# Kernel optimization log

Hardware: AMD Instinct MI355X
Metric: run time of the kernel (lower is better)

The kernel has to match this reference:

```python
import jax, jax.numpy as jnp
import numpy as np

BSZ, IN_DIM, OUT_DIM = 512, 1024, 2048
M_AND = 5        # Anderson memory (self.m)
BETA = 1.0
LAM = 1e-4
ALPHA = 1.0
TOL = 1e-5
MAX_ITER = 50
M_MON = 1.0      # monotonicity parameter of MONSingleFc


def _multiply(A, B, z):
    # MONSingleFc.multiply: (1-m)z - z A^T A + z B^T - z B
    Az = z @ A.T
    return (1.0 - M_MON) * z - Az @ A + z @ B.T - z @ B


def _relu(z):
    return jnp.maximum(z, 0.0)


def _single_it(A, B, z, bias):
    zn = _multiply(A, B, z)
    zn = (1.0 - ALPHA) * z + ALPHA * (zn + bias)
    zn = _relu(zn)
    err = jnp.linalg.norm(zn - z) / (1e-6 + jnp.linalg.norm(zn))
    return zn, err


def _anderson_solve(A, B, bias):
    bsz, d = bias.shape
    dt = bias.dtype
    Z = jnp.zeros((bsz, M_AND, d), dt)
    F = jnp.zeros((bsz, M_AND, d), dt)
    z0 = jnp.zeros((bsz, d), dt)
    f0, _ = _single_it(A, B, z0, bias)
    F = F.at[:, 0].set(f0)
    Z = Z.at[:, 1].set(f0)
    f1, _ = _single_it(A, B, f0, bias)
    F = F.at[:, 1].set(f1)
    eye = jnp.eye(M_AND, dtype=dt)

    def cond(s):
        Z, F, it, err = s
        return (it < MAX_ITER) & (err > TOL)

    def body(s):
        Z, F, it, _ = s
        n = jnp.minimum(M_AND, it)
        mask = jnp.arange(M_AND) < n                         # active Anderson slots
        # For it < m the unused slots of Z and F are still zero, so G = F - Z
        # has zero rows there and GGt's Frobenius norm matches the :n slice.
        G = F - Z                                            # (bsz, m, d)
        GGt = jnp.einsum('bmd,bnd->bmn', G, G)
        nrm = jnp.linalg.norm(GGt.reshape(GGt.shape[0], -1), axis=-1)
        GGt = GGt / (nrm[:, None, None] + 1e-6)
        pair = mask[:, None] & mask[None, :]
        # identity padding on inactive slots keeps the solve well-posed and
        # yields alpha = 0 there, equivalent to slicing [:n+1, :n+1].
        Hb = jnp.where(pair, GGt + LAM * eye, eye)
        mk = mask.astype(dt)
        H = jnp.zeros((bsz, M_AND + 1, M_AND + 1), dt)
        H = H.at[:, 0, 1:].set(mk).at[:, 1:, 0].set(mk).at[:, 1:, 1:].set(Hb)
        y = jnp.zeros((bsz, M_AND + 1, 1), dt).at[:, 0, 0].set(1.0)
        alpha = jnp.linalg.solve(H, y)[:, 1:, 0]             # (bsz, m)
        z_new = BETA * jnp.einsum('bm,bmd->bd', alpha, F) \
              + (1.0 - BETA) * jnp.einsum('bm,bmd->bd', alpha, Z)
        slot = it % M_AND
        Z = Z.at[:, slot].set(z_new)
        zo, err = _single_it(A, B, z_new, bias)
        F = F.at[:, slot].set(zo)
        return Z, F, it + 1, err

    Z, F, it, err = jax.lax.while_loop(
        cond, body, (Z, F, jnp.array(2, jnp.int32), jnp.array(jnp.inf, dt)))
    slot = (it - 1) % M_AND
    return Z[:, slot]


def setup_inputs():
    key = jax.random.key(0)
    kx, ka, kb, kw, kub = jax.random.split(key, 5)
    s = 1.0 / np.sqrt(OUT_DIM).astype(np.float32)
    x = jax.random.normal(kx, (BSZ, IN_DIM), jnp.float32)
    # scaled so ||W|| < 1 -> forward-backward splitting converges (trained MON regime)
    A = 0.3 * s * jax.random.normal(ka, (OUT_DIM, OUT_DIM), jnp.float32)
    B = 0.1 * s * jax.random.normal(kb, (OUT_DIM, OUT_DIM), jnp.float32)
    U_W = (1.0 / np.sqrt(IN_DIM).astype(np.float32)) * jax.random.normal(kw, (OUT_DIM, IN_DIM), jnp.float32)
    U_b = 0.01 * jax.random.normal(kub, (OUT_DIM,), jnp.float32)
    return {"x": x, "A": A, "B": B, "U_W": U_W, "U_b": U_b}


def reference(x, A, B, U_W, U_b):
    bias = x @ U_W.T + U_b                       # linear_module.bias(x)
    z_star = _anderson_solve(A, B, bias)         # equilibrium (no-grad in torch)
    zn = _relu(_multiply(A, B, z_star) + bias)   # final full step: nonlin(linear(x, z*))
    return zn
```

## Files before the change

kernel.cpp:

```cpp
#include <hip/hip_runtime.h>
#include <hip/hip_bf16.h>
#include <math.h>

#define BSZ      512
#define IN_DIM   1024
#define OUT_DIM  2048
#define M_AND    5
#define LAM      1e-4f
#define TOL      1e-5f
#define MAX_ITER 50
#define SPLIT_IT 24
#define NBLK     256

typedef __bf16 bf16x8 __attribute__((ext_vector_type(8)));
typedef float  f32x4  __attribute__((ext_vector_type(4)));
typedef unsigned short u16x8 __attribute__((ext_vector_type(8)));
typedef unsigned short u16x4 __attribute__((ext_vector_type(4)));
typedef __hip_bfloat16 bf16;

#define GAS __attribute__((address_space(1)))
#define LAS __attribute__((address_space(3)))

#define S_WAITCNT_VMCNT(N) asm volatile("s_waitcnt vmcnt(" #N ")" ::: "memory")

union BU { bf16 b; unsigned short u; };

__device__ __forceinline__ float bf2f(unsigned short u) {
    union { unsigned int i; float f; } c; c.i = (unsigned int)u << 16; return c.f;
}
__device__ __forceinline__ unsigned short f2bf(float f) {
    BU t; t.b = __float2bfloat16(f); return t.u;
}

static constexpr size_t BIAS_B = 0;
static constexpr size_t F_B    = BIAS_B + (size_t)BSZ * OUT_DIM * 4;
static constexpr size_t G_B    = F_B    + (size_t)BSZ * M_AND * OUT_DIM * 4;
static constexpr size_t ZH_B   = G_B    + (size_t)BSZ * M_AND * OUT_DIM * 2;
static constexpr size_t ZL_B   = ZH_B   + (size_t)BSZ * OUT_DIM * 2;
static constexpr size_t XH_B   = ZL_B   + (size_t)BSZ * OUT_DIM * 2;
static constexpr size_t XL_B   = XH_B   + (size_t)BSZ * IN_DIM * 2;
static constexpr size_t UH_B   = XL_B   + (size_t)BSZ * IN_DIM * 2;
static constexpr size_t UL_B   = UH_B   + (size_t)OUT_DIM * IN_DIM * 2;
static constexpr size_t AT_B   = UL_B   + (size_t)OUT_DIM * IN_DIM * 2;
static constexpr size_t WT_B   = AT_B   + (size_t)OUT_DIM * OUT_DIM * 2;
static constexpr size_t RED_B  = WT_B   + (size_t)OUT_DIM * OUT_DIM * 2;
static constexpr size_t BAR_B  = RED_B  + 512;
static constexpr size_t CTR_B  = BAR_B  + 64;
static constexpr size_t FLAG_B = CTR_B  + 256;
static constexpr size_t FSLOT_B = FLAG_B + 16;
static constexpr size_t CTRL_SZ = 512 + 64 + 256 + 16 + 16;

template<int ROUNDS>
__device__ __forceinline__ void stage_tile(const void* __restrict__ g0, int row_bytes,
                                           void* l0, int tid)
{
    #pragma unroll
    for (int q = 0; q < ROUNDS; ++q) {
        const int D   = q * 4096 + tid * 16;
        const int r   = D >> 7;
        const int cb  = D & 127;
        const int scb = cb ^ ((r & 7) << 4);
        const char* gsrc = (const char*)g0 + (size_t)r * row_bytes + scb;
        char* ldst = (char*)l0 + q * 4096 + (tid >> 6) * 1024;
        __builtin_amdgcn_global_load_lds((const GAS void*)gsrc, (LAS void*)ldst, 16, 0, 0);
    }
}

__device__ __forceinline__ bf16x8 read_frag(const void* tile, int row, int cb)
{
    return *(const bf16x8*)((const char*)tile + row * 128 + (cb ^ ((row & 7) << 4)));
}

__device__ __forceinline__ void gsync(unsigned int* bar)
{
    __syncthreads();
    if (threadIdx.x == 0) {
        __threadfence();
        const unsigned int g =
            __hip_atomic_load(&bar[1], __ATOMIC_ACQUIRE, __HIP_MEMORY_SCOPE_AGENT);
        const unsigned int a =
            __hip_atomic_fetch_add(&bar[0], 1u, __ATOMIC_ACQ_REL, __HIP_MEMORY_SCOPE_AGENT);
        if (a == NBLK - 1) {
            __hip_atomic_store(&bar[0], 0u, __ATOMIC_RELAXED, __HIP_MEMORY_SCOPE_AGENT);
            __hip_atomic_fetch_add(&bar[1], 1u, __ATOMIC_RELEASE, __HIP_MEMORY_SCOPE_AGENT);
        } else {
            while (__hip_atomic_load(&bar[1], __ATOMIC_ACQUIRE, __HIP_MEMORY_SCOPE_AGENT) == g)
                __builtin_amdgcn_s_sleep(1);
        }
        __threadfence();
    }
    __syncthreads();
}

__global__ __launch_bounds__(256)
void conv_hilo(const float* __restrict__ src, bf16* __restrict__ h, bf16* __restrict__ l)
{
    const size_t i4 = ((size_t)blockIdx.x * 256 + threadIdx.x) * 4;
    const float4 v = *(const float4*)&src[i4];
    const float vv[4] = {v.x, v.y, v.z, v.w};
    union { short4 s4; unsigned short u[4]; } ph, pl;
    #pragma unroll
    for (int j = 0; j < 4; ++j) {
        ph.u[j] = f2bf(vv[j]);
        pl.u[j] = f2bf(vv[j] - bf2f(ph.u[j]));
    }
    *(short4*)((char*)h + i4 * 2) = ph.s4;
    *(short4*)((char*)l + i4 * 2) = pl.s4;
}

__global__ __launch_bounds__(256)
void prep_at(const float* __restrict__ A, bf16* __restrict__ At)
{
    __shared__ float t[64][65];
    const int tid = threadIdx.x;
    const int k0 = blockIdx.y * 64, c0 = blockIdx.x * 64;
    const int cc = tid & 63, rr = tid >> 6;
    #pragma unroll
    for (int q = 0; q < 16; ++q)
        t[rr + 4 * q][cc] = A[(size_t)(k0 + rr + 4 * q) * OUT_DIM + c0 + cc];
    __syncthreads();
    #pragma unroll
    for (int q = 0; q < 16; ++q)
        At[(size_t)(c0 + rr + 4 * q) * OUT_DIM + k0 + cc] = __float2bfloat16(t[cc][rr + 4 * q]);
}

__global__ __launch_bounds__(256)
void w_mfma(const bf16* __restrict__ At, const float* __restrict__ Bm, bf16* __restrict__ Wt)
{
    __shared__ __align__(16) bf16 lds[2][2][64 * 64];
    const int tid = threadIdx.x;
    const int lane = tid & 63, wid = tid >> 6;
    const int wy = wid >> 1, wx = wid & 1;

    int bb = blockIdx.x;
    int ti = (int)((sqrtf(8.f * bb + 1.f) - 1.f) * 0.5f);
    while ((ti + 1) * (ti + 2) / 2 <= bb) ++ti;
    while (ti * (ti + 1) / 2 > bb) --ti;
    const int tj = bb - ti * (ti + 1) / 2;
    const int r0 = ti * 64, c0 = tj * 64;
    const bool diag = (ti == tj);

    f32x4 acc[2][2];
    #pragma unroll
    for (int i = 0; i < 2; ++i)
        #pragma unroll
        for (int j = 0; j < 2; ++j) acc[i][j] = 0;

    stage_tile<2>(At + (size_t)r0 * OUT_DIM, OUT_DIM * 2, lds[0][0], tid);
    stage_tile<2>(At + (size_t)c0 * OUT_DIM, OUT_DIM * 2, lds[0][1], tid);
    __syncthreads();
    int cur = 0;
    for (int t = 0; t < 32; ++t) {
        if (t + 1 < 32) {
            const int kk = (t + 1) * 64;
            stage_tile<2>(At + (size_t)r0 * OUT_DIM + kk, OUT_DIM * 2, lds[cur ^ 1][0], tid);
            stage_tile<2>(At + (size_t)c0 * OUT_DIM + kk, OUT_DIM * 2, lds[cur ^ 1][1], tid);
        }
        const bf16* Ta = lds[cur][0];
        const bf16* Tb = lds[cur][1];
        #pragma unroll
        for (int kf = 0; kf < 2; ++kf) {
            const int cb = kf * 64 + (lane >> 4) * 16;
            bf16x8 bfr[2];
            #pragma unroll
            for (int nj = 0; nj < 2; ++nj)
                bfr[nj] = read_frag(Tb, wx * 32 + nj * 16 + (lane & 15), cb);
            #pragma unroll
            for (int mi = 0; mi < 2; ++mi) {
                bf16x8 afr = read_frag(Ta, wy * 32 + mi * 16 + (lane & 15), cb);
                #pragma unroll
                for (int nj = 0; nj < 2; ++nj)
                    acc[mi][nj] = __builtin_amdgcn_mfma_f32_16x16x32_bf16(afr, bfr[nj], acc[mi][nj], 0, 0, 0);
            }
        }
        __syncthreads();
        cur ^= 1;
    }

    #pragma unroll
    for (int mi = 0; mi < 2; ++mi) {
        const int rb = r0 + wy * 32 + mi * 16 + (lane >> 4) * 4;
        #pragma unroll
        for (int nj = 0; nj < 2; ++nj) {
            const int c = c0 + wx * 32 + nj * 16 + (lane & 15);
            const float4 bc = *(const float4*)&Bm[(size_t)c * OUT_DIM + rb];
            const float bcv[4] = {bc.x, bc.y, bc.z, bc.w};
            union { short4 s4; unsigned short u[4]; } p;
            #pragma unroll
            for (int g = 0; g < 4; ++g) {
                const float a = acc[mi][nj][g];
                const float brc = Bm[(size_t)(rb + g) * OUT_DIM + c];
                const float w = bcv[g] - brc - a;
                p.u[g] = f2bf(w);
                if (!diag) {
                    const float wm = brc - bcv[g] - a;
                    *((unsigned short*)Wt + (size_t)(rb + g) * OUT_DIM + c) = f2bf(wm);
                }
            }
            *(short4*)((char*)Wt + ((size_t)c * OUT_DIM + rb) * 2) = p.s4;
        }
    }
}

__global__ __launch_bounds__(256)
void bias_mfma(const bf16* __restrict__ xh, const bf16* __restrict__ xl,
               const bf16* __restrict__ uh, const bf16* __restrict__ ul,
               const float* __restrict__ Ub, float* __restrict__ bias,
               float* __restrict__ F, unsigned short* __restrict__ G,
               unsigned short* __restrict__ zh, unsigned short* __restrict__ zl)
{
    __shared__ __align__(16) bf16 lds[2][4][64 * 64];
    const int tid = threadIdx.x;
    const int lane = tid & 63, wid = tid >> 6;
    const int wy = wid >> 1, wx = wid & 1;
    const int m0 = blockIdx.y * 64, n0 = blockIdx.x * 64;

    f32x4 acc[2][2];
    #pragma unroll
    for (int i = 0; i < 2; ++i)
        #pragma unroll
        for (int j = 0; j < 2; ++j) acc[i][j] = 0;

    stage_tile<2>(xh + (size_t)m0 * IN_DIM, IN_DIM * 2, lds[0][0], tid);
    stage_tile<2>(xl + (size_t)m0 * IN_DIM, IN_DIM * 2, lds[0][1], tid);
    stage_tile<2>(uh + (size_t)n0 * IN_DIM, IN_DIM * 2, lds[0][2], tid);
    stage_tile<2>(ul + (size_t)n0 * IN_DIM, IN_DIM * 2, lds[0][3], tid);
    __syncthreads();
    int cur = 0;
    for (int t = 0; t < 16; ++t) {
        if (t + 1 < 16) {
            const int kk = (t + 1) * 64;
            stage_tile<2>(xh + (size_t)m0 * IN_DIM + kk, IN_DIM * 2, lds[cur ^ 1][0], tid);
            stage_tile<2>(xl + (size_t)m0 * IN_DIM + kk, IN_DIM * 2, lds[cur ^ 1][1], tid);
            stage_tile<2>(uh + (size_t)n0 * IN_DIM + kk, IN_DIM * 2, lds[cur ^ 1][2], tid);
            stage_tile<2>(ul + (size_t)n0 * IN_DIM + kk, IN_DIM * 2, lds[cur ^ 1][3], tid);
        }
        const bf16* Txh = lds[cur][0];
        const bf16* Txl = lds[cur][1];
        const bf16* Tuh = lds[cur][2];
        const bf16* Tul = lds[cur][3];
        #pragma unroll
        for (int kf = 0; kf < 2; ++kf) {
            const int cb = kf * 64 + (lane >> 4) * 16;
            bf16x8 bh[2], bl[2];
            #pragma unroll
            for (int nj = 0; nj < 2; ++nj) {
                const int br = wx * 32 + nj * 16 + (lane & 15);
                bh[nj] = read_frag(Tuh, br, cb);
                bl[nj] = read_frag(Tul, br, cb);
            }
            #pragma unroll
            for (int mi = 0; mi < 2; ++mi) {
                const int ar = wy * 32 + mi * 16 + (lane & 15);
                bf16x8 ah = read_frag(Txh, ar, cb);
                bf16x8 al = read_frag(Txl, ar, cb);
                #pragma unroll
                for (int nj = 0; nj < 2; ++nj) {
                    acc[mi][nj] = __builtin_amdgcn_mfma_f32_16x16x32_bf16(ah, bh[nj], acc[mi][nj], 0, 0, 0);
                    acc[mi][nj] = __builtin_amdgcn_mfma_f32_16x16x32_bf16(ah, bl[nj], acc[mi][nj], 0, 0, 0);
                    acc[mi][nj] = __builtin_amdgcn_mfma_f32_16x16x32_bf16(al, bh[nj], acc[mi][nj], 0, 0, 0);
                }
            }
        }
        __syncthreads();
        cur ^= 1;
    }

    #pragma unroll
    for (int mi = 0; mi < 2; ++mi) {
        const int mb = m0 + wy * 32 + mi * 16 + (lane >> 4) * 4;
        #pragma unroll
        for (int nj = 0; nj < 2; ++nj) {
            const int n = n0 + wx * 32 + nj * 16 + (lane & 15);
            const float ub = Ub[n];
            #pragma unroll
            for (int g = 0; g < 4; ++g) {
                const int m = mb + g;
                const size_t idx = (size_t)m * OUT_DIM + n;
                const float v = acc[mi][nj][g] + ub;
                bias[idx] = v;
                const float f = fmaxf(v, 0.f);
                F[((size_t)m * M_AND + 0) * OUT_DIM + n] = f;
                G[((size_t)m * M_AND + 0) * OUT_DIM + n] = f2bf(f);
                const unsigned short h = f2bf(f);
                zh[idx] = h;
                zl[idx] = f2bf(f - bf2f(h));
            }
        }
    }
}

template<bool DO_ERR>
__device__ __forceinline__ void iter_core(
    const int m0, const int n0, const int tid,
    const unsigned short* __restrict__ zh, const unsigned short* __restrict__ zl,
    const bf16* __restrict__ Wt, const float* __restrict__ bias,
    float* __restrict__ F, unsigned short* __restrict__ G,
    float* red, bf16* lds_buf, const int slot, const int it)
{
    const int lane = tid & 63, wid = tid >> 6;
    const int wy = wid >> 1, wx = wid & 1;
    #define BUFP(s,i) (lds_buf + ((s) * 3 + (i)) * 4096)

    f32x4 acc[2][2];
    #pragma unroll
    for (int i = 0; i < 2; ++i)
        #pragma unroll
        for (int j = 0; j < 2; ++j) acc[i][j] = 0;

    auto STAGE = [&](int s, int kk) {
        stage_tile<2>(zh + (size_t)m0 * OUT_DIM + kk, OUT_DIM * 2, BUFP(s, 0), tid);
        stage_tile<2>(zl + (size_t)m0 * OUT_DIM + kk, OUT_DIM * 2, BUFP(s, 1), tid);
        stage_tile<2>(Wt + (size_t)n0 * OUT_DIM + kk, OUT_DIM * 2, BUFP(s, 2), tid);
    };

    STAGE(0, 0);
    STAGE(1, 64);
    for (int t = 0; t < 32; ++t) {
        const int s = t % 3;
        if (t + 2 < 32) { S_WAITCNT_VMCNT(6); } else { S_WAITCNT_VMCNT(0); }
        __builtin_amdgcn_s_barrier();
        if (t + 2 < 32) STAGE((t + 2) % 3, (t + 2) * 64);
        const bf16* Th = BUFP(s, 0);
        const bf16* Tl = BUFP(s, 1);
        const bf16* Tw = BUFP(s, 2);
        #pragma unroll
        for (int kf = 0; kf < 2; ++kf) {
            const int cb = kf * 64 + (lane >> 4) * 16;
            bf16x8 bfr[2];
            #pragma unroll
            for (int nj = 0; nj < 2; ++nj)
                bfr[nj] = read_frag(Tw, wx * 32 + nj * 16 + (lane & 15), cb);
            #pragma unroll
            for (int mi = 0; mi < 2; ++mi) {
                const int rrow = wy * 32 + mi * 16 + (lane & 15);
                bf16x8 ah = read_frag(Th, rrow, cb);
                bf16x8 al = read_frag(Tl, rrow, cb);
                #pragma unroll
                for (int nj = 0; nj < 2; ++nj) {
                    acc[mi][nj] = __builtin_amdgcn_mfma_f32_16x16x32_bf16(ah, bfr[nj], acc[mi][nj], 0, 0, 0);
                    acc[mi][nj] = __builtin_amdgcn_mfma_f32_16x16x32_bf16(al, bfr[nj], acc[mi][nj], 0, 0, 0);
                }
            }
        }
    }
    #undef BUFP

    float lnum = 0.f, lden = 0.f;
    #pragma unroll
    for (int mi = 0; mi < 2; ++mi) {
        const int mb = m0 + wy * 32 + mi * 16 + (lane >> 4) * 4;
        #pragma unroll
        for (int nj = 0; nj < 2; ++nj) {
            const int n = n0 + wx * 32 + nj * 16 + (lane & 15);
            #pragma unroll
            for (int g = 0; g < 4; ++g) {
                const int m = mb + g;
                const size_t idx = (size_t)m * OUT_DIM + n;
                float v = acc[mi][nj][g] + bias[idx];
                v = fmaxf(v, 0.f);
                const float zc = bf2f(zh[idx]) + bf2f(zl[idx]);
                const float gg = v - zc;
                F[((size_t)m * M_AND + slot) * OUT_DIM + n] = v;
                G[((size_t)m * M_AND + slot) * OUT_DIM + n] = f2bf(gg);
                if (DO_ERR) { lnum += gg * gg; lden += v * v; }
            }
        }
    }

    if (DO_ERR) {
        #pragma unroll
        for (int off = 32; off; off >>= 1) {
            lnum += __shfl_down(lnum, off);
            lden += __shfl_down(lden, off);
        }
        __shared__ float swn[4], swd[4];
        if ((tid & 63) == 0) { swn[tid >> 6] = lnum; swd[tid >> 6] = lden; }
        __syncthreads();
        if (tid == 0) {
            atomicAdd(&red[2 * it],     swn[0] + swn[1] + swn[2] + swn[3]);
            atomicAdd(&red[2 * it + 1], swd[0] + swd[1] + swd[2] + swd[3]);
        }
    }
}

__device__ __forceinline__ void swz_mn(int bid, int& m0, int& n0)
{
    const int xcd = bid & 7, sl = bid >> 3;
    n0 = (xcd * 4 + (sl & 3)) * 64;
    m0 = (sl >> 2) * 64;
}

template<bool DO_ERR>
__global__ __launch_bounds__(256)
void iter_mfma(const unsigned short* __restrict__ zh, const unsigned short* __restrict__ zl,
               const bf16* __restrict__ Wt, const float* __restrict__ bias,
               float* __restrict__ F, unsigned short* __restrict__ G,
               float* red, unsigned int* ctr, int* flag, int* fslot, int slot, int it)
{
    if (((volatile int*)flag)[0]) return;
    __shared__ __align__(16) bf16 lds_buf[3 * 3 * 4096];
    int m0, n0;
    swz_mn(blockIdx.x, m0, n0);
    iter_core<DO_ERR>(m0, n0, threadIdx.x, zh, zl, Wt, bias, F, G, red, lds_buf, slot, it);
    if (DO_ERR && threadIdx.x == 0) {
        __threadfence();
        const unsigned int done = atomicAdd(&ctr[it], 1u);
        if (done == 256 - 1) {
            ((volatile int*)fslot)[0] = slot;
            const float num2 = ((volatile float*)red)[2 * it];
            const float den2 = ((volatile float*)red)[2 * it + 1];
            if (sqrtf(num2) <= TOL * (1e-6f + sqrtf(den2)))
                ((volatile int*)flag)[0] = 1;
        }
    }
}

__global__ __launch_bounds__(256)
void final_copy(const float* __restrict__ F, const int* __restrict__ fslot,
                float* __restrict__ out)
{
    const int s = ((volatile const int*)fslot)[0];
    const size_t i4 = ((size_t)blockIdx.x * 256 + threadIdx.x) * 4;
    const int m = (int)(i4 >> 11), n = (int)(i4 & 2047);
    *(float4*)&out[i4] = *(const float4*)&F[((size_t)m * M_AND + s) * OUT_DIM + n];
}

__global__ __launch_bounds__(512)
void anderson_kernel(const float* __restrict__ F, const unsigned short* __restrict__ G,
                     unsigned short* __restrict__ zh, unsigned short* __restrict__ zl,
                     int* flag, int it)
{
    if (((volatile int*)flag)[0]) return;
    const int b = blockIdx.x;
    const int tid = threadIdx.x;
    const int lane = tid & 63, wid = tid >> 6;
    const int n = (it < M_AND) ? it : M_AND;
    const int c0 = tid * 4;
    const unsigned short* Gb = G + (size_t)b * M_AND * OUT_DIM;
    const float* Fb = F + (size_t)b * M_AND * OUT_DIM;

    float g[M_AND][4];
    float4 f[M_AND];
    #pragma unroll
    for (int m = 0; m < M_AND; ++m) {
        f[m] = *(const float4*)(Fb + (size_t)m * OUT_DIM + c0);
        if (m < n) {
            const u16x4 gv = *(const u16x4*)(Gb + (size_t)m * OUT_DIM + c0);
            #pragma unroll
            for (int q = 0; q < 4; ++q) g[m][q] = bf2f(gv[q]);
        } else {
            #pragma unroll
            for (int q = 0; q < 4; ++q) g[m][q] = 0.f;
        }
    }

    float dots[15];
    {
        int p = 0;
        #pragma unroll
        for (int i = 0; i < M_AND; ++i)
            #pragma unroll
            for (int j = i; j < M_AND; ++j) {
                float s = 0.f;
                #pragma unroll
                for (int q = 0; q < 4; ++q) s += g[i][q] * g[j][q];
                dots[p++] = s;
            }
    }

    __shared__ float sred[15][8];
    #pragma unroll
    for (int p = 0; p < 15; ++p) {
        float v = dots[p];
        #pragma unroll
        for (int off = 32; off; off >>= 1) v += __shfl_xor(v, off);
        if (lane == 0) sred[p][wid] = v;
    }
    __syncthreads();

    __shared__ float s_alpha[M_AND];
    if (tid == 0) {
        float GGm[M_AND][M_AND];
        int p = 0;
        for (int i = 0; i < M_AND; ++i)
            for (int j = i; j < M_AND; ++j) {
                float v = 0.f;
                for (int w = 0; w < 8; ++w) v += sred[p][w];
                GGm[i][j] = v; GGm[j][i] = v; ++p;
            }
        float fro = 0.f;
        for (int i = 0; i < M_AND; ++i)
            for (int j = 0; j < M_AND; ++j) fro += GGm[i][j] * GGm[i][j];
        const float inv = 1.f / (sqrtf(fro) + 1e-6f);

        float Mm[M_AND][M_AND];
        for (int i = 0; i < n; ++i)
            for (int j = 0; j < n; ++j)
                Mm[i][j] = GGm[i][j] * inv + (i == j ? LAM : 0.f);

        float L[M_AND][M_AND];
        for (int i = 0; i < n; ++i)
            for (int j = 0; j <= i; ++j) {
                float s = Mm[i][j];
                for (int k = 0; k < j; ++k) s -= L[i][k] * L[j][k];
                L[i][j] = (i == j) ? sqrtf(fmaxf(s, 1e-20f)) : s / L[j][j];
            }
        float y[M_AND], u[M_AND];
        for (int i = 0; i < n; ++i) {
            float s = 1.f;
            for (int k = 0; k < i; ++k) s -= L[i][k] * y[k];
            y[i] = s / L[i][i];
        }
        for (int i = n - 1; i >= 0; --i) {
            float s = y[i];
            for (int k = i + 1; k < n; ++k) s -= L[k][i] * u[k];
            u[i] = s / L[i][i];
        }
        float su = 0.f;
        for (int i = 0; i < n; ++i) su += u[i];
        const float isu = 1.f / su;
        for (int m = 0; m < M_AND; ++m) s_alpha[m] = (m < n) ? u[m] * isu : 0.f;
    }
    __syncthreads();

    float z[4] = {};
    #pragma unroll
    for (int m = 0; m < M_AND; ++m) {
        if (m < n) {
            const float a = s_alpha[m];
            z[0] += a * f[m].x; z[1] += a * f[m].y;
            z[2] += a * f[m].z; z[3] += a * f[m].w;
        }
    }
    u16x4 hv, lv;
    #pragma unroll
    for (int q = 0; q < 4; ++q) {
        const unsigned short h = f2bf(z[q]);
        hv[q] = h;
        lv[q] = f2bf(z[q] - bf2f(h));
    }
    *(u16x4*)(zh + (size_t)b * OUT_DIM + c0) = hv;
    *(u16x4*)(zl + (size_t)b * OUT_DIM + c0) = lv;
}

__global__ __launch_bounds__(256)
void tail_loop(unsigned short* zh, unsigned short* zl,
               const bf16* __restrict__ Wt, const float* __restrict__ bias,
               float* F, unsigned short* G,
               float* red, unsigned int* bar, int* flag, int* fslot)
{
    if (((volatile int*)flag)[0]) return;
    __shared__ __align__(16) bf16 lds_buf[3 * 3 * 4096];
    __shared__ float sred2[2][2][15];
    __shared__ float s_alpha[2][M_AND];
    const int bid = blockIdx.x, tid = threadIdx.x;
    int m0, n0;
    swz_mn(bid, m0, n0);

    for (int it = SPLIT_IT; it < MAX_ITER; ++it) {
        {
            const int half = tid >> 7, lt = tid & 127;
            const int r = bid * 2 + half;
            const int wv = lt >> 6;
            const unsigned short* Gb = G + (size_t)r * M_AND * OUT_DIM;
            const float* Fb = F + (size_t)r * M_AND * OUT_DIM;
            const int c0 = lt * 16;

            float g[M_AND][16];
            #pragma unroll
            for (int m = 0; m < M_AND; ++m) {
                const u16x8 ga = *(const u16x8*)(Gb + (size_t)m * OUT_DIM + c0);
                const u16x8 gb2 = *(const u16x8*)(Gb + (size_t)m * OUT_DIM + c0 + 8);
                #pragma unroll
                for (int q = 0; q < 8; ++q) { g[m][q] = bf2f(ga[q]); g[m][8 + q] = bf2f(gb2[q]); }
            }
            {
                int p = 0;
                #pragma unroll
                for (int i = 0; i < M_AND; ++i)
                    #pragma unroll
                    for (int j = i; j < M_AND; ++j) {
                        float s = 0.f;
                        #pragma unroll
                        for (int q = 0; q < 16; ++q) s += g[i][q] * g[j][q];
                        float v = s;
                        #pragma unroll
                        for (int off = 32; off; off >>= 1) v += __shfl_xor(v, off);
                        if ((lt & 63) == 0) sred2[half][wv][p] = v;
                        ++p;
                    }
            }
            __syncthreads();
            if (lt == 0) {
                float GGm[M_AND][M_AND];
                int p = 0;
                for (int i = 0; i < M_AND; ++i)
                    for (int j = i; j < M_AND; ++j) {
                        const float v = sred2[half][0][p] + sred2[half][1][p];
                        GGm[i][j] = v; GGm[j][i] = v; ++p;
                    }
                float fro = 0.f;
                for (int i = 0; i < M_AND; ++i)
                    for (int j = 0; j < M_AND; ++j) fro += GGm[i][j] * GGm[i][j];
                const float inv = 1.f / (sqrtf(fro) + 1e-6f);
                float Mm[M_AND][M_AND];
                for (int i = 0; i < M_AND; ++i)
                    for (int j = 0; j < M_AND; ++j)
                        Mm[i][j] = GGm[i][j] * inv + (i == j ? LAM : 0.f);
                float L[M_AND][M_AND];
                for (int i = 0; i < M_AND; ++i)
                    for (int j = 0; j <= i; ++j) {
                        float s = Mm[i][j];
                        for (int k = 0; k < j; ++k) s -= L[i][k] * L[j][k];
                        L[i][j] = (i == j) ? sqrtf(fmaxf(s, 1e-20f)) : s / L[j][j];
                    }
                float y[M_AND], u[M_AND];
                for (int i = 0; i < M_AND; ++i) {
                    float s = 1.f;
                    for (int k = 0; k < i; ++k) s -= L[i][k] * y[k];
                    y[i] = s / L[i][i];
                }
                for (int i = M_AND - 1; i >= 0; --i) {
                    float s = y[i];
                    for (int k = i + 1; k < M_AND; ++k) s -= L[k][i] * u[k];
                    u[i] = s / L[i][i];
                }
                float su = 0.f;
                for (int i = 0; i < M_AND; ++i) su += u[i];
                const float isu = 1.f / su;
                for (int m = 0; m < M_AND; ++m) s_alpha[half][m] = u[m] * isu;
            }
            __syncthreads();
            float z[16] = {};
            for (int m = 0; m < M_AND; ++m) {
                const float a = s_alpha[half][m];
                #pragma unroll
                for (int q = 0; q < 4; ++q) {
                    const float4 fv = *(const float4*)(Fb + (size_t)m * OUT_DIM + c0 + q * 4);
                    z[q * 4 + 0] += a * fv.x; z[q * 4 + 1] += a * fv.y;
                    z[q * 4 + 2] += a * fv.z; z[q * 4 + 3] += a * fv.w;
                }
            }
            u16x8 hv[2], lv[2];
            #pragma unroll
            for (int q = 0; q < 16; ++q) {
                const unsigned short h = f2bf(z[q]);
                hv[q >> 3][q & 7] = h;
                lv[q >> 3][q & 7] = f2bf(z[q] - bf2f(h));
            }
            const size_t base = (size_t)r * OUT_DIM + c0;
            *(u16x8*)(zh + base)     = hv[0];
            *(u16x8*)(zh + base + 8) = hv[1];
            *(u16x8*)(zl + base)     = lv[0];
            *(u16x8*)(zl + base + 8) = lv[1];
        }
        gsync(bar);
        iter_core<true>(m0, n0, tid, zh, zl, Wt, bias, F, G, red, lds_buf, it % M_AND, it);
        gsync(bar);
        if (bid == 0 && tid == 0) ((volatile int*)fslot)[0] = it % M_AND;
        const float num2 = __hip_atomic_load(&red[2 * it], __ATOMIC_RELAXED, __HIP_MEMORY_SCOPE_AGENT);
        const float den2 = __hip_atomic_load(&red[2 * it + 1], __ATOMIC_RELAXED, __HIP_MEMORY_SCOPE_AGENT);
        if (sqrtf(num2) <= TOL * (1e-6f + sqrtf(den2))) break;
    }
}

extern "C" void kernel_launch(void* const* d_in, const int* in_sizes, int n_in,
                              void* d_out, int out_size, void* d_ws, size_t ws_size,
                              hipStream_t stream)
{
    const float* x  = (const float*)d_in[0];
    const float* A  = (const float*)d_in[1];
    const float* B  = (const float*)d_in[2];
    const float* UW = (const float*)d_in[3];
    const float* Ub = (const float*)d_in[4];
    float* out = (float*)d_out;
    char*  wsb = (char*)d_ws;

    float*          bias = (float*)(wsb + BIAS_B);
    float*          F    = (float*)(wsb + F_B);
    unsigned short* G    = (unsigned short*)(wsb + G_B);
    unsigned short* zh   = (unsigned short*)(wsb + ZH_B);
    unsigned short* zl   = (unsigned short*)(wsb + ZL_B);
    bf16*           xh   = (bf16*)(wsb + XH_B);
    bf16*           xl   = (bf16*)(wsb + XL_B);
    bf16*           uh   = (bf16*)(wsb + UH_B);
    bf16*           ul   = (bf16*)(wsb + UL_B);
    bf16*           At   = (bf16*)(wsb + AT_B);
    bf16*           Wt   = (bf16*)(wsb + WT_B);
    float*          red  = (float*)(wsb + RED_B);
    unsigned int*   bar  = (unsigned int*)(wsb + BAR_B);
    unsigned int*   ctr  = (unsigned int*)(wsb + CTR_B);
    int*            flag = (int*)(wsb + FLAG_B);
    int*            fslot= (int*)(wsb + FSLOT_B);

    hipMemsetAsync(wsb + RED_B, 0, CTRL_SZ, stream);

    conv_hilo<<<dim3(BSZ * IN_DIM / 1024),     256, 0, stream>>>(x,  xh, xl);
    conv_hilo<<<dim3(OUT_DIM * IN_DIM / 1024), 256, 0, stream>>>(UW, uh, ul);
    prep_at  <<<dim3(32, 32), 256, 0, stream>>>(A, At);
    w_mfma   <<<dim3(528), 256, 0, stream>>>(At, B, Wt);
    bias_mfma<<<dim3(32, 8), 256, 0, stream>>>(xh, xl, uh, ul, Ub, bias, F, G, zh, zl);

    iter_mfma<false><<<dim3(NBLK), 256, 0, stream>>>(zh, zl, Wt, bias, F, G,
                                                     red, ctr, flag, fslot, 1, 0);

    for (int it = 2; it < SPLIT_IT; ++it) {
        anderson_kernel<<<dim3(BSZ), 512, 0, stream>>>(F, G, zh, zl, flag, it);
        iter_mfma<true><<<dim3(NBLK), 256, 0, stream>>>(zh, zl, Wt, bias, F, G,
                                                        red, ctr, flag, fslot, it % M_AND, it);
    }
    tail_loop<<<dim3(NBLK), 256, 0, stream>>>(zh, zl, Wt, bias, F, G, red, bar, flag, fslot);
    final_copy<<<dim3(BSZ * OUT_DIM / 1024), 256, 0, stream>>>(F, fslot, out);
}
```

Measured before the change: 569.9 us.

## Halve iteration GEMM tile M to launch 512 blocks and add MFMA priority

Shrinks the per-block output tile of the fixed-point iteration GEMM from 64x64 to 32x64, doubling the grid to 512 blocks so more of the 256 CUs have two resident workgroups and can overlap latency. The persistent tail loop now has each of its 256 blocks process two tiles sequentially. s_setprio is raised around the MFMA section. The cost is that each block reuses its staged Wt tile over fewer rows, so more global and LDS traffic goes to reloading weights. The tail loop also gets two serialized GEMM passes per block.

Result: slower. 602.2 us (+5.7%).

```diff
diff --git a/kernel.cpp b/kernel.cpp
--- a/kernel.cpp
+++ b/kernel.cpp
@@ -11,6 +11,7 @@
 #define MAX_ITER 50
 #define SPLIT_IT 24
 #define NBLK     256
+#define ITERBLK  512
 
 typedef __bf16 bf16x8 __attribute__((ext_vector_type(8)));
 typedef float  f32x4  __attribute__((ext_vector_type(4)));
@@ -300,71 +301,60 @@
 {
     const int lane = tid & 63, wid = tid >> 6;
     const int wy = wid >> 1, wx = wid & 1;
-    #define BUFP(s,i) (lds_buf + ((s) * 3 + (i)) * 4096)
-
-    f32x4 acc[2][2];
-    #pragma unroll
-    for (int i = 0; i < 2; ++i)
-        #pragma unroll
-        for (int j = 0; j < 2; ++j) acc[i][j] = 0;
+    #define BUFP(s) (lds_buf + (s) * 8192)
+
+    f32x4 acc[2];
+    acc[0] = 0; acc[1] = 0;
 
     auto STAGE = [&](int s, int kk) {
-        stage_tile<2>(zh + (size_t)m0 * OUT_DIM + kk, OUT_DIM * 2, BUFP(s, 0), tid);
-        stage_tile<2>(zl + (size_t)m0 * OUT_DIM + kk, OUT_DIM * 2, BUFP(s, 1), tid);
-        stage_tile<2>(Wt + (size_t)n0 * OUT_DIM + kk, OUT_DIM * 2, BUFP(s, 2), tid);
+        stage_tile<1>(zh + (size_t)m0 * OUT_DIM + kk, OUT_DIM * 2, BUFP(s), tid);
+        stage_tile<1>(zl + (size_t)m0 * OUT_DIM + kk, OUT_DIM * 2, BUFP(s) + 2048, tid);
+        stage_tile<2>(Wt + (size_t)n0 * OUT_DIM + kk, OUT_DIM * 2, BUFP(s) + 4096, tid);
     };
 
     STAGE(0, 0);
     STAGE(1, 64);
     for (int t = 0; t < 32; ++t) {
         const int s = t % 3;
-        if (t + 2 < 32) { S_WAITCNT_VMCNT(6); } else { S_WAITCNT_VMCNT(0); }
+        if (t + 2 < 32) { S_WAITCNT_VMCNT(4); } else { S_WAITCNT_VMCNT(0); }
         __builtin_amdgcn_s_barrier();
         if (t + 2 < 32) STAGE((t + 2) % 3, (t + 2) * 64);
-        const bf16* Th = BUFP(s, 0);
-        const bf16* Tl = BUFP(s, 1);
-        const bf16* Tw = BUFP(s, 2);
+        const bf16* Th = BUFP(s);
+        const bf16* Tl = BUFP(s) + 2048;
+        const bf16* Tw = BUFP(s) + 4096;
+        __builtin_amdgcn_s_setprio(1);
         #pragma unroll
         for (int kf = 0; kf < 2; ++kf) {
             const int cb = kf * 64 + (lane >> 4) * 16;
-            bf16x8 bfr[2];
-            #pragma unroll
-            for (int nj = 0; nj < 2; ++nj)
-                bfr[nj] = read_frag(Tw, wx * 32 + nj * 16 + (lane & 15), cb);
-            #pragma unroll
-            for (int mi = 0; mi < 2; ++mi) {
-                const int rrow = wy * 32 + mi * 16 + (lane & 15);
-                bf16x8 ah = read_frag(Th, rrow, cb);
-                bf16x8 al = read_frag(Tl, rrow, cb);
-                #pragma unroll
-                for (int nj = 0; nj < 2; ++nj) {
-                    acc[mi][nj] = __builtin_amdgcn_mfma_f32_16x16x32_bf16(ah, bfr[nj], acc[mi][nj], 0, 0, 0);
-                    acc[mi][nj] = __builtin_amdgcn_mfma_f32_16x16x32_bf16(al, bfr[nj], acc[mi][nj], 0, 0, 0);
-                }
-            }
-        }
+            bf16x8 b0 = read_frag(Tw, wx * 32 + (lane & 15), cb);
+            bf16x8 b1 = read_frag(Tw, wx * 32 + 16 + (lane & 15), cb);
+            bf16x8 ah = read_frag(Th, wy * 16 + (lane & 15), cb);
+            bf16x8 al = read_frag(Tl, wy * 16 + (lane & 15), cb);
+            acc[0] = __builtin_amdgcn_mfma_f32_16x16x32_bf16(ah, b0, acc[0], 0, 0, 0);
+            acc[0] = __builtin_amdgcn_mfma_f32_16x16x32_bf16(al, b0, acc[0], 0, 0, 0);
+            acc[1] = __builtin_amdgcn_mfma_f32_16x16x32_bf16(ah, b1, acc[1], 0, 0, 0);
+            acc[1] = __builtin_amdgcn_mfma_f32_16x16x32_bf16(al, b1, acc[1], 0, 0, 0);
+        }
+        __builtin_amdgcn_s_setprio(0);
     }
     #undef BUFP
 
     float lnum = 0.f, lden = 0.f;
-    #pragma unroll
-    for (int mi = 0; mi < 2; ++mi) {
-        const int mb = m0 + wy * 32 + mi * 16 + (lane >> 4) * 4;
-        #pragma unroll
-        for (int nj = 0; nj < 2; ++nj) {
-            const int n = n0 + wx * 32 + nj * 16 + (lane & 15);
-            #pragma unroll
-            for (int g = 0; g < 4; ++g) {
-                const int m = mb + g;
-                const size_t idx = (size_t)m * OUT_DIM + n;
-                float v = acc[mi][nj][g] + bias[idx];
-                v = fmaxf(v, 0.f);
-                const float zc = bf2f(zh[idx]) + bf2f(zl[idx]);
-                const float gg = v - zc;
-                F[((size_t)m * M_AND + slot) * OUT_DIM + n] = v;
-                G[((size_t)m * M_AND + slot) * OUT_DIM + n] = f2bf(gg);
-                if (DO_ERR) { lnum += gg * gg; lden += v * v; }
-            }
+    const int mb = m0 + wy * 16 + (lane >> 4) * 4;
+    #pragma unroll
+    for (int nj = 0; nj < 2; ++nj) {
+        const int n = n0 + wx * 32 + nj * 16 + (lane & 15);
+        #pragma unroll
+        for (int g = 0; g < 4; ++g) {
+            const int m = mb + g;
+            const size_t idx = (size_t)m * OUT_DIM + n;
+            float v = acc[nj][g] + bias[idx];
+            v = fmaxf(v, 0.f);
+            const float zc = bf2f(zh[idx]) + bf2f(zl[idx]);
+            const float gg = v - zc;
+            F[((size_t)m * M_AND + slot) * OUT_DIM + n] = v;
+            G[((size_t)m * M_AND + slot) * OUT_DIM + n] = f2bf(gg);
+            if (DO_ERR) { lnum += gg * gg; lden += v * v; }
         }
     }
 
@@ -388,7 +378,7 @@
 {
     const int xcd = bid & 7, sl = bid >> 3;
     n0 = (xcd * 4 + (sl & 3)) * 64;
-    m0 = (sl >> 2) * 64;
+    m0 = (sl >> 2) * 32;
 }
 
 template<bool DO_ERR>
@@ -399,14 +389,14 @@
                float* red, unsigned int* ctr, int* flag, int* fslot, int slot, int it)
 {
     if (((volatile int*)flag)[0]) return;
-    __shared__ __align__(16) bf16 lds_buf[3 * 3 * 4096];
+    __shared__ __align__(16) bf16 lds_buf[3 * 8192];
     int m0, n0;
     swz_mn(blockIdx.x, m0, n0);
     iter_core<DO_ERR>(m0, n0, threadIdx.x, zh, zl, Wt, bias, F, G, red, lds_buf, slot, it);
     if (DO_ERR && threadIdx.x == 0) {
         __threadfence();
         const unsigned int done = atomicAdd(&ctr[it], 1u);
-        if (done == 256 - 1) {
+        if (done == ITERBLK - 1) {
             ((volatile int*)fslot)[0] = slot;
             const float num2 = ((volatile float*)red)[2 * it];
             const float den2 = ((volatile float*)red)[2 * it + 1];
@@ -551,12 +541,13 @@
                float* red, unsigned int* bar, int* flag, int* fslot)
 {
     if (((volatile int*)flag)[0]) return;
-    __shared__ __align__(16) bf16 lds_buf[3 * 3 * 4096];
+    __shared__ __align__(16) bf16 lds_buf[3 * 8192];
     __shared__ float sred2[2][2][15];
     __shared__ float s_alpha[2][M_AND];
     const int bid = blockIdx.x, tid = threadIdx.x;
-    int m0, n0;
-    swz_mn(bid, m0, n0);
+    int m0a, n0a, m0b, n0b;
+    swz_mn(bid, m0a, n0a);
+    swz_mn(bid + 256, m0b, n0b);
 
     for (int it = SPLIT_IT; it < MAX_ITER; ++it) {
         {
@@ -656,7 +647,8 @@
             *(u16x8*)(zl + base + 8) = lv[1];
         }
         gsync(bar);
-        iter_core<true>(m0, n0, tid, zh, zl, Wt, bias, F, G, red, lds_buf, it % M_AND, it);
+        iter_core<true>(m0a, n0a, tid, zh, zl, Wt, bias, F, G, red, lds_buf, it % M_AND, it);
+        iter_core<true>(m0b, n0b, tid, zh, zl, Wt, bias, F, G, red, lds_buf, it % M_AND, it);
         gsync(bar);
         if (bid == 0 && tid == 0) ((volatile int*)fslot)[0] = it % M_AND;
         const float num2 = __hip_atomic_load(&red[2 * it], __ATOMIC_RELAXED, __HIP_MEMORY_SCOPE_AGENT);
@@ -702,13 +694,13 @@
     w_mfma   <<<dim3(528), 256, 0, stream>>>(At, B, Wt);
     bias_mfma<<<dim3(32, 8), 256, 0, stream>>>(xh, xl, uh, ul, Ub, bias, F, G, zh, zl);
 
-    iter_mfma<false><<<dim3(NBLK), 256, 0, stream>>>(zh, zl, Wt, bias, F, G,
-                                                     red, ctr, flag, fslot, 1, 0);
+    iter_mfma<false><<<dim3(ITERBLK), 256, 0, stream>>>(zh, zl, Wt, bias, F, G,
+                                                        red, ctr, flag, fslot, 1, 0);
 
     for (int it = 2; it < SPLIT_IT; ++it) {
         anderson_kernel<<<dim3(BSZ), 512, 0, stream>>>(F, G, zh, zl, flag, it);
-        iter_mfma<true><<<dim3(NBLK), 256, 0, stream>>>(zh, zl, Wt, bias, F, G,
-                                                        red, ctr, flag, fslot, it % M_AND, it);
+        iter_mfma<true><<<dim3(ITERBLK), 256, 0, stream>>>(zh, zl, Wt, bias, F, G,
+                                                           red, ctr, flag, fslot, it % M_AND, it);
     }
     tail_loop<<<dim3(NBLK), 256, 0, stream>>>(zh, zl, Wt, bias, F, G, red, bar, flag, fslot);
     final_copy<<<dim3(BSZ * OUT_DIM / 1024), 256, 0, stream>>>(F, fslot, out);
```

## Replace LDS-staged GEMM with direct global-to-register fragment pipeline

Applied to the files above, without the earlier changes.

The per-iteration GEMM core no longer stages z-hi, z-lo and weight tiles through a triple-buffered LDS ring guarded by barriers. Each wave now loads its MFMA fragments straight from global memory into registers, using a four-deep software pipeline and s_setprio around the MFMA groups. Dropping the shared-memory buffers removes block barriers and LDS traffic and may raise occupancy, at the cost of more VGPRs and uncoalesced, L2-dependent loads with no reuse across waves. It also moves the switch to the persistent tail loop earlier (SPLIT_IT 24→16) and skips loading F rows for inactive Anderson slots.

After: 685.3 us. +20.2%, slower.

```diff
diff --git a/kernel.cpp b/kernel.cpp
--- a/kernel.cpp
+++ b/kernel.cpp
@@ -9,7 +9,7 @@
 #define LAM      1e-4f
 #define TOL      1e-5f
 #define MAX_ITER 50
-#define SPLIT_IT 24
+#define SPLIT_IT 16
 #define NBLK     256
 
 typedef __bf16 bf16x8 __attribute__((ext_vector_type(8)));
@@ -20,8 +20,6 @@
 
 #define GAS __attribute__((address_space(1)))
 #define LAS __attribute__((address_space(3)))
-
-#define S_WAITCNT_VMCNT(N) asm volatile("s_waitcnt vmcnt(" #N ")" ::: "memory")
 
 union BU { bf16 b; unsigned short u; };
 
@@ -290,17 +288,46 @@
     }
 }
 
+struct FS { bf16x8 ah0, ah1, al0, al1, b0, b1; };
+
+__device__ __forceinline__ void fs_load(FS& f, const char* zhb, const char* zlb,
+                                        const char* wtb, const size_t lo, const int kb)
+{
+    f.ah0 = *(const bf16x8*)(zhb + kb + lo);
+    f.ah1 = *(const bf16x8*)(zhb + kb + lo + 16 * 4096);
+    f.al0 = *(const bf16x8*)(zlb + kb + lo);
+    f.al1 = *(const bf16x8*)(zlb + kb + lo + 16 * 4096);
+    f.b0  = *(const bf16x8*)(wtb + kb + lo);
+    f.b1  = *(const bf16x8*)(wtb + kb + lo + 16 * 4096);
+}
+
+__device__ __forceinline__ void fs_mma(const FS& f, f32x4 acc[2][2])
+{
+    acc[0][0] = __builtin_amdgcn_mfma_f32_16x16x32_bf16(f.ah0, f.b0, acc[0][0], 0, 0, 0);
+    acc[0][0] = __builtin_amdgcn_mfma_f32_16x16x32_bf16(f.al0, f.b0, acc[0][0], 0, 0, 0);
+    acc[0][1] = __builtin_amdgcn_mfma_f32_16x16x32_bf16(f.ah0, f.b1, acc[0][1], 0, 0, 0);
+    acc[0][1] = __builtin_amdgcn_mfma_f32_16x16x32_bf16(f.al0, f.b1, acc[0][1], 0, 0, 0);
+    acc[1][0] = __builtin_amdgcn_mfma_f32_16x16x32_bf16(f.ah1, f.b0, acc[1][0], 0, 0, 0);
+    acc[1][0] = __builtin_amdgcn_mfma_f32_16x16x32_bf16(f.al1, f.b0, acc[1][0], 0, 0, 0);
+    acc[1][1] = __builtin_amdgcn_mfma_f32_16x16x32_bf16(f.ah1, f.b1, acc[1][1], 0, 0, 0);
+    acc[1][1] = __builtin_amdgcn_mfma_f32_16x16x32_bf16(f.al1, f.b1, acc[1][1], 0, 0, 0);
+}
+
 template<bool DO_ERR>
 __device__ __forceinline__ void iter_core(
     const int m0, const int n0, const int tid,
     const unsigned short* __restrict__ zh, const unsigned short* __restrict__ zl,
     const bf16* __restrict__ Wt, const float* __restrict__ bias,
     float* __restrict__ F, unsigned short* __restrict__ G,
-    float* red, bf16* lds_buf, const int slot, const int it)
+    float* red, const int slot, const int it)
 {
     const int lane = tid & 63, wid = tid >> 6;
-    const int wy = wid >> 1, wx = wid & 1;
-    #define BUFP(s,i) (lds_buf + ((s) * 3 + (i)) * 4096)
+    const int wm = (wid >> 1) * 32, wn = (wid & 1) * 32;
+
+    const char* zhb = (const char*)zh + (size_t)(m0 + wm) * 4096;
+    const char* zlb = (const char*)zl + (size_t)(m0 + wm) * 4096;
+    const char* wtb = (const char*)Wt + (size_t)(n0 + wn) * 4096;
+    const size_t lo = (size_t)(lane & 15) * 4096 + (size_t)((lane >> 4) * 16);
 
     f32x4 acc[2][2];
     #pragma unroll
@@ -308,56 +335,42 @@
         #pragma unroll
         for (int j = 0; j < 2; ++j) acc[i][j] = 0;
 
-    auto STAGE = [&](int s, int kk) {
-        stage_tile<2>(zh + (size_t)m0 * OUT_DIM + kk, OUT_DIM * 2, BUFP(s, 0), tid);
-        stage_tile<2>(zl + (size_t)m0 * OUT_DIM + kk, OUT_DIM * 2, BUFP(s, 1), tid);
-        stage_tile<2>(Wt + (size_t)n0 * OUT_DIM + kk, OUT_DIM * 2, BUFP(s, 2), tid);
-    };
-
-    STAGE(0, 0);
-    STAGE(1, 64);
-    for (int t = 0; t < 32; ++t) {
-        const int s = t % 3;
-        if (t + 2 < 32) { S_WAITCNT_VMCNT(6); } else { S_WAITCNT_VMCNT(0); }
-        __builtin_amdgcn_s_barrier();
-        if (t + 2 < 32) STAGE((t + 2) % 3, (t + 2) * 64);
-        const bf16* Th = BUFP(s, 0);
-        const bf16* Tl = BUFP(s, 1);
-        const bf16* Tw = BUFP(s, 2);
-        #pragma unroll
-        for (int kf = 0; kf < 2; ++kf) {
-            const int cb = kf * 64 + (lane >> 4) * 16;
-            bf16x8 bfr[2];
-            #pragma unroll
-            for (int nj = 0; nj < 2; ++nj)
-                bfr[nj] = read_frag(Tw, wx * 32 + nj * 16 + (lane & 15), cb);
-            #pragma unroll
-            for (int mi = 0; mi < 2; ++mi) {
-                const int rrow = wy * 32 + mi * 16 + (lane & 15);
-                bf16x8 ah = read_frag(Th, rrow, cb);
-                bf16x8 al = read_frag(Tl, rrow, cb);
-                #pragma unroll
-                for (int nj = 0; nj < 2; ++nj) {
-                    acc[mi][nj] = __builtin_amdgcn_mfma_f32_16x16x32_bf16(ah, bfr[nj], acc[mi][nj], 0, 0, 0);
-                    acc[mi][nj] = __builtin_amdgcn_mfma_f32_16x16x32_bf16(al, bfr[nj], acc[mi][nj], 0, 0, 0);
-                }
-            }
-        }
-    }
-    #undef BUFP
+    FS fA, fB, fC, fD;
+    fs_load(fA, zhb, zlb, wtb, lo, 0);
+    fs_load(fB, zhb, zlb, wtb, lo, 64);
+    fs_load(fC, zhb, zlb, wtb, lo, 128);
+    fs_load(fD, zhb, zlb, wtb, lo, 192);
+    for (int kb = 0; kb < 4096; kb += 256) {
+        __builtin_amdgcn_s_setprio(1);
+        fs_mma(fA, acc);
+        __builtin_amdgcn_s_setprio(0);
+        if (kb + 256 < 4096) fs_load(fA, zhb, zlb, wtb, lo, kb + 256);
+        __builtin_amdgcn_s_setprio(1);
+        fs_mma(fB, acc);
+        __builtin_amdgcn_s_setprio(0);
+        if (kb + 320 < 4096) fs_load(fB, zhb, zlb, wtb, lo, kb + 320);
+        __builtin_amdgcn_s_setprio(1);
+        fs_mma(fC, acc);
+        __builtin_amdgcn_s_setprio(0);
+        if (kb + 384 < 4096) fs_load(fC, zhb, zlb, wtb, lo, kb + 384);
+        __builtin_amdgcn_s_setprio(1);
+        fs_mma(fD, acc);
+        __builtin_amdgcn_s_setprio(0);
+        if (kb + 448 < 4096) fs_load(fD, zhb, zlb, wtb, lo, kb + 448);
+    }
 
     float lnum = 0.f, lden = 0.f;
     #pragma unroll
-    for (int mi = 0; mi < 2; ++mi) {
-        const int mb = m0 + wy * 32 + mi * 16 + (lane >> 4) * 4;
-        #pragma unroll
-        for (int nj = 0; nj < 2; ++nj) {
-            const int n = n0 + wx * 32 + nj * 16 + (lane & 15);
+    for (int i = 0; i < 2; ++i) {
+        const int mb = m0 + wm + i * 16 + (lane >> 4) * 4;
+        #pragma unroll
+        for (int j = 0; j < 2; ++j) {
+            const int n = n0 + wn + j * 16 + (lane & 15);
             #pragma unroll
             for (int g = 0; g < 4; ++g) {
                 const int m = mb + g;
                 const size_t idx = (size_t)m * OUT_DIM + n;
-                float v = acc[mi][nj][g] + bias[idx];
+                float v = acc[i][j][g] + bias[idx];
                 v = fmaxf(v, 0.f);
                 const float zc = bf2f(zh[idx]) + bf2f(zl[idx]);
                 const float gg = v - zc;
@@ -399,14 +412,13 @@
                float* red, unsigned int* ctr, int* flag, int* fslot, int slot, int it)
 {
     if (((volatile int*)flag)[0]) return;
-    __shared__ __align__(16) bf16 lds_buf[3 * 3 * 4096];
     int m0, n0;
     swz_mn(blockIdx.x, m0, n0);
-    iter_core<DO_ERR>(m0, n0, threadIdx.x, zh, zl, Wt, bias, F, G, red, lds_buf, slot, it);
+    iter_core<DO_ERR>(m0, n0, threadIdx.x, zh, zl, Wt, bias, F, G, red, slot, it);
     if (DO_ERR && threadIdx.x == 0) {
         __threadfence();
         const unsigned int done = atomicAdd(&ctr[it], 1u);
-        if (done == 256 - 1) {
+        if (done == NBLK - 1) {
             ((volatile int*)fslot)[0] = slot;
             const float num2 = ((volatile float*)red)[2 * it];
             const float den2 = ((volatile float*)red)[2 * it + 1];
@@ -444,12 +456,13 @@
     float4 f[M_AND];
     #pragma unroll
     for (int m = 0; m < M_AND; ++m) {
-        f[m] = *(const float4*)(Fb + (size_t)m * OUT_DIM + c0);
         if (m < n) {
+            f[m] = *(const float4*)(Fb + (size_t)m * OUT_DIM + c0);
             const u16x4 gv = *(const u16x4*)(Gb + (size_t)m * OUT_DIM + c0);
             #pragma unroll
             for (int q = 0; q < 4; ++q) g[m][q] = bf2f(gv[q]);
         } else {
+            f[m] = float4{0.f, 0.f, 0.f, 0.f};
             #pragma unroll
             for (int q = 0; q < 4; ++q) g[m][q] = 0.f;
         }
@@ -551,7 +564,6 @@
                float* red, unsigned int* bar, int* flag, int* fslot)
 {
     if (((volatile int*)flag)[0]) return;
-    __shared__ __align__(16) bf16 lds_buf[3 * 3 * 4096];
     __shared__ float sred2[2][2][15];
     __shared__ float s_alpha[2][M_AND];
     const int bid = blockIdx.x, tid = threadIdx.x;
@@ -656,7 +668,7 @@
             *(u16x8*)(zl + base + 8) = lv[1];
         }
         gsync(bar);
-        iter_core<true>(m0, n0, tid, zh, zl, Wt, bias, F, G, red, lds_buf, it % M_AND, it);
+        iter_core<true>(m0, n0, tid, zh, zl, Wt, bias, F, G, red, it % M_AND, it);
         gsync(bar);
         if (bid == 0 && tid == 0) ((volatile int*)fslot)[0] = it % M_AND;
         const float num2 = __hip_atomic_load(&red[2 * it], __ATOMIC_RELAXED, __HIP_MEMORY_SCOPE_AGENT);
```
